# Optimization experiments

Hardware: AMD Instinct MI355X
Metric: run time of the kernel (lower is better)

The kernel has to match this reference:

```python
import jax, jax.numpy as jnp
import numpy as np

B, N, E, H, D, F = 2, 4096, 128, 8, 16, 512
EPS = 1e-6


def _rms_norm(x, w):
    xf = x.astype(jnp.float32)
    n = xf * jax.lax.rsqrt(jnp.mean(xf * xf, axis=-1, keepdims=True) + EPS)
    return n.astype(x.dtype) * w


def setup_inputs() -> dict:
    key = jax.random.key(0)
    ks = jax.random.split(key, 12)
    s = 1.0 / np.sqrt(E)
    sf = 1.0 / np.sqrt(F)
    coords = jax.random.uniform(ks[10], (B, N, 2))
    dis = jnp.sqrt(jnp.sum((coords[:, :, None, :] - coords[:, None, :, :]) ** 2, -1))
    dis = dis * (1.0 - jnp.eye(N))  # zero diagonal
    return {
        "input1": jax.random.normal(ks[0], (B, N, E), jnp.float32),
        "dis_matrix": dis.astype(jnp.float32),
        "Wq": jax.random.uniform(ks[1], (E, E), jnp.float32, -s, s),
        "Wk": jax.random.uniform(ks[2], (E, E), jnp.float32, -s, s),
        "Wv": jax.random.uniform(ks[3], (E, E), jnp.float32, -s, s),
        "alpha": jnp.float32(1.0),
        "ln1_w": jnp.ones((E,), jnp.float32),
        "ln2_w": jnp.ones((E,), jnp.float32),
        "Wcomb": jax.random.uniform(ks[4], (E, E), jnp.float32, -s, s),
        "W1": jax.random.uniform(ks[5], (F, E), jnp.float32, -s, s),
        "b1": jax.random.uniform(ks[6], (F,), jnp.float32, -s, s),
        "W2": jax.random.uniform(ks[7], (E, F), jnp.float32, -sf, sf),
        "b2": jax.random.uniform(ks[8], (E,), jnp.float32, -sf, sf),
    }


def _sparse_attention_afm(x, dis_matrix, Wq, Wk, Wv, alpha):
    # project and split heads: [B,N,E] -> [B,H,N,D]
    def heads(w):
        return (x @ w.T).reshape(B, N, H, D).transpose(0, 2, 1, 3)
    q, k, v = heads(Wq), heads(Wk), heads(Wv)
    log2n = jnp.float32(np.log2(N))
    dis_weight = jnp.exp(-alpha * log2n * dis_matrix)  # [B,N,N] (i,j)
    k_weight = jnp.exp(k)  # [B,H,N,D]
    w1 = jnp.einsum('bij,bhik->bhjk', dis_weight, k_weight * v)
    w2 = jnp.einsum('bij,bhik->bhjk', dis_weight, k_weight)
    out = jax.nn.sigmoid(q) * (w1 / w2)  # [B,H,N,D]
    return out.transpose(0, 2, 1, 3).reshape(B, N, E)


def reference(input1, dis_matrix, Wq, Wk, Wv, alpha, ln1_w, ln2_w, Wcomb, W1, b1, W2, b2):
    h = _rms_norm(input1, ln1_w)
    attn = _sparse_attention_afm(h, dis_matrix, Wq, Wk, Wv, alpha)
    out1 = input1 + attn @ Wcomb.T
    h2 = _rms_norm(out1, ln2_w)
    ffn = jax.nn.relu(h2 @ W1.T + b1) @ W2.T + b2
    return out1 + ffn
```

## Files before the change

### kernel.cpp

```cpp
#include <hip/hip_runtime.h>

#define NTOK 4096
#define BNROWS 8192
#define EDIM 128
#define FDIM 512

typedef __attribute__((ext_vector_type(8))) short bf16x8;
typedef __attribute__((ext_vector_type(4))) float f32x4;

__device__ __forceinline__ ushort f2bf(float x) {
    union { float f; unsigned u; } c; c.f = x;
    unsigned r = c.u + 0x7FFF + ((c.u >> 16) & 1);
    return (ushort)(r >> 16);
}

__launch_bounds__(256, 1)
__global__ void qkv_k(const float* __restrict__ input1, const float* __restrict__ ln1w,
                      const float* __restrict__ Wq, const float* __restrict__ Wk,
                      const float* __restrict__ Wv, const float* __restrict__ Wc,
                      const float* __restrict__ W1, const float* __restrict__ W2,
                      ushort* __restrict__ Wbf, float* __restrict__ sigq,
                      ushort* __restrict__ Mt) {
    const int bx = blockIdx.x, t = threadIdx.x;
    if (bx >= 256) {
        int off = (bx - 256) * 1024 + t * 4;
        const float* src; int o2;
        if (off < 16384)      { src = Wc; o2 = off; }
        else if (off < 81920) { src = W1; o2 = off - 16384; }
        else                  { src = W2; o2 = off - 81920; }
        float4 f = *(const float4*)(src + o2);
        ushort4 u; u.x = f2bf(f.x); u.y = f2bf(f.y); u.z = f2bf(f.z); u.w = f2bf(f.w);
        *(ushort4*)(Wbf + off) = u;
        return;
    }
    __shared__ ushort As[32 * 136];
    __shared__ ushort Bs[3][128 * 136];
    const int lane = t & 63, wv = t >> 6;
    const int m15 = lane & 15, quad = lane >> 4, kq = quad * 8;
    const int M0 = bx * 32;

    {
        const int ar = t >> 3, c0 = (t & 7) * 16;
        const float* xr = input1 + (size_t)(M0 + ar) * EDIM + c0;
        float4 x[4];
        float ss = 0.f;
#pragma unroll
        for (int i = 0; i < 4; ++i) {
            x[i] = ((const float4*)xr)[i];
            ss += x[i].x * x[i].x + x[i].y * x[i].y + x[i].z * x[i].z + x[i].w * x[i].w;
        }
        ss += __shfl_down(ss, 4, 8);
        ss += __shfl_down(ss, 2, 8);
        ss += __shfl_down(ss, 1, 8);
        ss = __shfl(ss, 0, 8);
        float rr = rsqrtf(ss * (1.0f / 128.0f) + 1e-6f);
#pragma unroll
        for (int i = 0; i < 4; ++i) {
            float4 wv4 = *(const float4*)&ln1w[c0 + i * 4];
            ushort4 o;
            o.x = f2bf(x[i].x * rr * wv4.x);
            o.y = f2bf(x[i].y * rr * wv4.y);
            o.z = f2bf(x[i].z * rr * wv4.z);
            o.w = f2bf(x[i].w * rr * wv4.w);
            *(ushort4*)&As[ar * 136 + c0 + i * 4] = o;
        }
    }
    {
        const int br = t >> 1, half = (t & 1) * 64;
        const float* srcs[3] = {Wq, Wk, Wv};
#pragma unroll
        for (int m = 0; m < 3; ++m) {
            const float* wsrc = srcs[m] + (size_t)br * 128 + half;
#pragma unroll
            for (int j = 0; j < 8; ++j) {
                float4 f0 = *(const float4*)(wsrc + j * 8);
                float4 f1 = *(const float4*)(wsrc + j * 8 + 4);
                bf16x8 u;
                u[0] = (short)f2bf(f0.x); u[1] = (short)f2bf(f0.y);
                u[2] = (short)f2bf(f0.z); u[3] = (short)f2bf(f0.w);
                u[4] = (short)f2bf(f1.x); u[5] = (short)f2bf(f1.y);
                u[6] = (short)f2bf(f1.z); u[7] = (short)f2bf(f1.w);
                *(bf16x8*)&Bs[m][br * 136 + half + j * 8] = u;
            }
        }
    }
    __syncthreads();

    f32x4 aq[2][2] = {}, ak[2][2] = {}, av[2][2] = {};
    const int c0w = wv * 32;
#pragma unroll
    for (int kc = 0; kc < 4; ++kc) {
        int ko = kc * 32 + kq;
        bf16x8 a0 = *(const bf16x8*)&As[m15 * 136 + ko];
        bf16x8 a1 = *(const bf16x8*)&As[(16 + m15) * 136 + ko];
#pragma unroll
        for (int ni = 0; ni < 2; ++ni) {
            int brow = (c0w + ni * 16 + m15) * 136 + ko;
            bf16x8 bq = *(const bf16x8*)&Bs[0][brow];
            bf16x8 bk = *(const bf16x8*)&Bs[1][brow];
            bf16x8 bv = *(const bf16x8*)&Bs[2][brow];
            aq[0][ni] = __builtin_amdgcn_mfma_f32_16x16x32_bf16(a0, bq, aq[0][ni], 0, 0, 0);
            aq[1][ni] = __builtin_amdgcn_mfma_f32_16x16x32_bf16(a1, bq, aq[1][ni], 0, 0, 0);
            ak[0][ni] = __builtin_amdgcn_mfma_f32_16x16x32_bf16(a0, bk, ak[0][ni], 0, 0, 0);
            ak[1][ni] = __builtin_amdgcn_mfma_f32_16x16x32_bf16(a1, bk, ak[1][ni], 0, 0, 0);
            av[0][ni] = __builtin_amdgcn_mfma_f32_16x16x32_bf16(a0, bv, av[0][ni], 0, 0, 0);
            av[1][ni] = __builtin_amdgcn_mfma_f32_16x16x32_bf16(a1, bv, av[1][ni], 0, 0, 0);
        }
    }
    const int b  = M0 >> 12;
    const int i0 = M0 & (NTOK - 1);
#pragma unroll
    for (int mi = 0; mi < 2; ++mi)
#pragma unroll
        for (int ni = 0; ni < 2; ++ni) {
            int e  = c0w + ni * 16 + m15;
            int ib = i0 + mi * 16 + quad * 4;
#pragma unroll
            for (int r = 0; r < 4; ++r)
                sigq[(size_t)(M0 + mi * 16 + quad * 4 + r) * EDIM + e] =
                    1.0f / (1.0f + __expf(-aq[mi][ni][r]));
            ushort4 pv, pk;
            float k0 = __expf(ak[mi][ni][0]); pv.x = f2bf(k0 * av[mi][ni][0]); pk.x = f2bf(k0);
            float k1 = __expf(ak[mi][ni][1]); pv.y = f2bf(k1 * av[mi][ni][1]); pk.y = f2bf(k1);
            float k2 = __expf(ak[mi][ni][2]); pv.z = f2bf(k2 * av[mi][ni][2]); pk.z = f2bf(k2);
            float k3 = __expf(ak[mi][ni][3]); pv.w = f2bf(k3 * av[mi][ni][3]); pk.w = f2bf(k3);
            *(ushort4*)&Mt[((size_t)b * 256 + e) * NTOK + ib]       = pv;
            *(ushort4*)&Mt[((size_t)b * 256 + 128 + e) * NTOK + ib] = pk;
        }
}

__launch_bounds__(256, 3)
__global__ void big_gemm_k(const float* __restrict__ dis, const float* __restrict__ alphap,
                           const ushort* __restrict__ Mt, float* __restrict__ P) {
    __shared__ ushort As[32 * 72];
    __shared__ ushort Bs[256 * 72];
    const int t = threadIdx.x, lane = t & 63, wv = t >> 6;
    const int m15 = lane & 15, quad = lane >> 4, kq = quad * 8;
    const int j0 = blockIdx.x * 32;
    const int b  = blockIdx.y;
    const int s  = blockIdx.z;
    const float coef = -alphap[0] * 12.0f;
    const float* disb = dis + (size_t)b * NTOK * NTOK;
    const ushort* Mtb = Mt + (size_t)b * 256 * NTOK;
    float* outp = P + ((size_t)(s * 2 + b) * NTOK + j0) * 256;

    f32x4 acc[2][4] = {};
    const int aj = t >> 3, ak = (t & 7) * 8;
    const int brow = t >> 3, bseg = (t & 7) * 8;
    const int k0 = s * (NTOK / 4);
    const int nIter = (NTOK / 4) / 64;

    float4 fa0, fa1;
    bf16x8 pb[8];
    {
        const float* ap = disb + (size_t)(j0 + aj) * NTOK + k0 + ak;
        fa0 = *(const float4*)ap; fa1 = *(const float4*)(ap + 4);
#pragma unroll
        for (int p = 0; p < 8; ++p)
            pb[p] = *(const bf16x8*)&Mtb[(size_t)(p * 32 + brow) * NTOK + k0 + bseg];
    }

    for (int it = 0; it < nIter; ++it) {
        bf16x8 a8;
        a8[0] = (short)f2bf(__expf(coef * fa0.x));
        a8[1] = (short)f2bf(__expf(coef * fa0.y));
        a8[2] = (short)f2bf(__expf(coef * fa0.z));
        a8[3] = (short)f2bf(__expf(coef * fa0.w));
        a8[4] = (short)f2bf(__expf(coef * fa1.x));
        a8[5] = (short)f2bf(__expf(coef * fa1.y));
        a8[6] = (short)f2bf(__expf(coef * fa1.z));
        a8[7] = (short)f2bf(__expf(coef * fa1.w));
        *(bf16x8*)&As[aj * 72 + ak] = a8;
#pragma unroll
        for (int p = 0; p < 8; ++p)
            *(bf16x8*)&Bs[(p * 32 + brow) * 72 + bseg] = pb[p];
        __syncthreads();
        if (it < nIter - 1) {
            int kn = k0 + (it + 1) * 64;
            const float* ap = disb + (size_t)(j0 + aj) * NTOK + kn + ak;
            fa0 = *(const float4*)ap; fa1 = *(const float4*)(ap + 4);
#pragma unroll
            for (int p = 0; p < 8; ++p)
                pb[p] = *(const bf16x8*)&Mtb[(size_t)(p * 32 + brow) * NTOK + kn + bseg];
        }
#pragma unroll
        for (int kh = 0; kh < 2; ++kh) {
            int ko = kh * 32 + kq;
            bf16x8 a0 = *(const bf16x8*)&As[m15 * 72 + ko];
            bf16x8 a1 = *(const bf16x8*)&As[(16 + m15) * 72 + ko];
#pragma unroll
            for (int ni = 0; ni < 4; ++ni) {
                bf16x8 bv = *(const bf16x8*)&Bs[(wv * 64 + ni * 16 + m15) * 72 + ko];
                acc[0][ni] = __builtin_amdgcn_mfma_f32_16x16x32_bf16(a0, bv, acc[0][ni], 0, 0, 0);
                acc[1][ni] = __builtin_amdgcn_mfma_f32_16x16x32_bf16(a1, bv, acc[1][ni], 0, 0, 0);
            }
        }
        __syncthreads();
    }
#pragma unroll
    for (int mi = 0; mi < 2; ++mi)
#pragma unroll
        for (int ni = 0; ni < 4; ++ni)
#pragma unroll
            for (int r = 0; r < 4; ++r) {
                int j = mi * 16 + quad * 4 + r;
                int c = wv * 64 + ni * 16 + m15;
                outp[(size_t)j * 256 + c] = acc[mi][ni][r];
            }
}

__launch_bounds__(256, 2)
__global__ void wcomb_rms2_k(const float* __restrict__ sigq, const float* __restrict__ P,
                             const ushort* __restrict__ Wbf,
                             const float* __restrict__ input1, const float* __restrict__ b2,
                             const float* __restrict__ ln2w,
                             float* __restrict__ outD, ushort* __restrict__ h2) {
    __shared__ ushort As[32 * 136];
    __shared__ ushort Bs[128 * 136];
    __shared__ float  O[32][132];
    const int t = threadIdx.x, lane = t & 63, wv = t >> 6;
    const int m15 = lane & 15, quad = lane >> 4, kq = quad * 8;
    const int M0 = blockIdx.x * 32;

    {
        const int ar = t >> 3, e0 = (t & 7) * 16;
        const int g = M0 + ar;
        const int b = g >> 12, j = g & (NTOK - 1);
        const float* sg = sigq + (size_t)g * 128 + e0;
        const float* Pg0 = P + ((size_t)(0 + b) * NTOK + j) * 256 + e0;
        const float* Pg1 = P + ((size_t)(2 + b) * NTOK + j) * 256 + e0;
        const float* Pg2 = P + ((size_t)(4 + b) * NTOK + j) * 256 + e0;
        const float* Pg3 = P + ((size_t)(6 + b) * NTOK + j) * 256 + e0;
#pragma unroll
        for (int i = 0; i < 4; ++i) {
            float4 s = *(const float4*)(sg + i * 4);
            float4 n0 = *(const float4*)(Pg0 + i * 4);
            float4 n1 = *(const float4*)(Pg1 + i * 4);
            float4 n2 = *(const float4*)(Pg2 + i * 4);
            float4 n3 = *(const float4*)(Pg3 + i * 4);
            float4 d0 = *(const float4*)(Pg0 + 128 + i * 4);
            float4 d1 = *(const float4*)(Pg1 + 128 + i * 4);
            float4 d2 = *(const float4*)(Pg2 + 128 + i * 4);
            float4 d3 = *(const float4*)(Pg3 + 128 + i * 4);
            ushort4 a;
            a.x = f2bf(s.x * (n0.x + n1.x + n2.x + n3.x) / (d0.x + d1.x + d2.x + d3.x));
            a.y = f2bf(s.y * (n0.y + n1.y + n2.y + n3.y) / (d0.y + d1.y + d2.y + d3.y));
            a.z = f2bf(s.z * (n0.z + n1.z + n2.z + n3.z) / (d0.z + d1.z + d2.z + d3.z));
            a.w = f2bf(s.w * (n0.w + n1.w + n2.w + n3.w) / (d0.w + d1.w + d2.w + d3.w));
            *(ushort4*)&As[ar * 136 + e0 + i * 4] = a;
        }
    }
    {
        const int br = t >> 1, half = (t & 1) * 64;
#pragma unroll
        for (int j = 0; j < 8; ++j)
            *(bf16x8*)&Bs[br * 136 + half + j * 8] =
                *(const bf16x8*)&Wbf[(size_t)br * 128 + half + j * 8];
    }
    __syncthreads();

    f32x4 acc[2][2] = {};
    const int c0w = wv * 32;
#pragma unroll
    for (int kc = 0; kc < 4; ++kc) {
        int ko = kc * 32 + kq;
        bf16x8 a0 = *(const bf16x8*)&As[m15 * 136 + ko];
        bf16x8 a1 = *(const bf16x8*)&As[(16 + m15) * 136 + ko];
        bf16x8 b0 = *(const bf16x8*)&Bs[(c0w + m15) * 136 + ko];
        bf16x8 b1 = *(const bf16x8*)&Bs[(c0w + 16 + m15) * 136 + ko];
        acc[0][0] = __builtin_amdgcn_mfma_f32_16x16x32_bf16(a0, b0, acc[0][0], 0, 0, 0);
        acc[0][1] = __builtin_amdgcn_mfma_f32_16x16x32_bf16(a0, b1, acc[0][1], 0, 0, 0);
        acc[1][0] = __builtin_amdgcn_mfma_f32_16x16x32_bf16(a1, b0, acc[1][0], 0, 0, 0);
        acc[1][1] = __builtin_amdgcn_mfma_f32_16x16x32_bf16(a1, b1, acc[1][1], 0, 0, 0);
    }
#pragma unroll
    for (int mi = 0; mi < 2; ++mi)
#pragma unroll
        for (int ni = 0; ni < 2; ++ni)
#pragma unroll
            for (int r = 0; r < 4; ++r) {
                int rl = mi * 16 + quad * 4 + r;
                int col = c0w + ni * 16 + m15;
                size_t off = (size_t)(M0 + rl) * 128 + col;
                float v = acc[mi][ni][r] + input1[off];
                O[rl][col] = v;
                outD[off] = v + b2[col];
            }
    __syncthreads();
    {
        const int row = t >> 3, seg = t & 7;
        float4 x[4];
        float ss = 0.f;
#pragma unroll
        for (int i = 0; i < 4; ++i) {
            x[i] = *(const float4*)&O[row][seg * 16 + i * 4];
            ss += x[i].x * x[i].x + x[i].y * x[i].y + x[i].z * x[i].z + x[i].w * x[i].w;
        }
        ss += __shfl_down(ss, 4, 8);
        ss += __shfl_down(ss, 2, 8);
        ss += __shfl_down(ss, 1, 8);
        ss = __shfl(ss, 0, 8);
        float rr = rsqrtf(ss * (1.0f / 128.0f) + 1e-6f);
        ushort* hp = h2 + (size_t)(M0 + row) * 128 + seg * 16;
#pragma unroll
        for (int i = 0; i < 4; ++i) {
            float4 wv4 = *(const float4*)&ln2w[seg * 16 + i * 4];
            ushort4 o;
            o.x = f2bf(x[i].x * rr * wv4.x);
            o.y = f2bf(x[i].y * rr * wv4.y);
            o.z = f2bf(x[i].z * rr * wv4.z);
            o.w = f2bf(x[i].w * rr * wv4.w);
            *(ushort4*)&hp[i * 4] = o;
        }
    }
}

__launch_bounds__(256, 2)
__global__ void ffn_k(const ushort* __restrict__ h2, const ushort* __restrict__ Wbf,
                      const float* __restrict__ b1, float* __restrict__ out) {
    __shared__ ushort As[32 * 136];
    __shared__ ushort Am[32 * 520];
    __shared__ ushort Bs[128 * 136];
    const int t = threadIdx.x, lane = t & 63, wv = t >> 6;
    const int m15 = lane & 15, quad = lane >> 4, kq = quad * 8;
    const int M0 = blockIdx.x * 32;
    const int c0w = wv * 32;
    const int br = t >> 1, half = (t & 1) * 64;
    const ushort* W1bf = Wbf + 16384;
    const ushort* W2bf = Wbf + 81920;

    {
        const int ar = t >> 3, a0 = (t & 7) * 16;
        *(bf16x8*)&As[ar * 136 + a0]     = *(const bf16x8*)&h2[(size_t)(M0 + ar) * 128 + a0];
        *(bf16x8*)&As[ar * 136 + a0 + 8] = *(const bf16x8*)&h2[(size_t)(M0 + ar) * 128 + a0 + 8];
    }
    for (int fc = 0; fc < 4; ++fc) {
        __syncthreads();
#pragma unroll
        for (int j = 0; j < 8; ++j)
            *(bf16x8*)&Bs[br * 136 + half + j * 8] =
                *(const bf16x8*)&W1bf[(size_t)(fc * 128 + br) * 128 + half + j * 8];
        __syncthreads();
        f32x4 acc[2][2] = {};
#pragma unroll
        for (int kc = 0; kc < 4; ++kc) {
            int ko = kc * 32 + kq;
            bf16x8 a0 = *(const bf16x8*)&As[m15 * 136 + ko];
            bf16x8 a1 = *(const bf16x8*)&As[(16 + m15) * 136 + ko];
            bf16x8 b0 = *(const bf16x8*)&Bs[(c0w + m15) * 136 + ko];
            bf16x8 b1v = *(const bf16x8*)&Bs[(c0w + 16 + m15) * 136 + ko];
            acc[0][0] = __builtin_amdgcn_mfma_f32_16x16x32_bf16(a0, b0, acc[0][0], 0, 0, 0);
            acc[0][1] = __builtin_amdgcn_mfma_f32_16x16x32_bf16(a0, b1v, acc[0][1], 0, 0, 0);
            acc[1][0] = __builtin_amdgcn_mfma_f32_16x16x32_bf16(a1, b0, acc[1][0], 0, 0, 0);
            acc[1][1] = __builtin_amdgcn_mfma_f32_16x16x32_bf16(a1, b1v, acc[1][1], 0, 0, 0);
        }
#pragma unroll
        for (int mi = 0; mi < 2; ++mi)
#pragma unroll
            for (int ni = 0; ni < 2; ++ni)
#pragma unroll
                for (int r = 0; r < 4; ++r) {
                    int row = mi * 16 + quad * 4 + r;
                    int col = c0w + ni * 16 + m15;
                    Am[row * 520 + fc * 128 + col] =
                        f2bf(fmaxf(acc[mi][ni][r] + b1[fc * 128 + col], 0.0f));
                }
    }
    f32x4 acc2[2][2] = {};
    for (int kc = 0; kc < 4; ++kc) {
        __syncthreads();
#pragma unroll
        for (int j = 0; j < 8; ++j)
            *(bf16x8*)&Bs[br * 136 + half + j * 8] =
                *(const bf16x8*)&W2bf[(size_t)br * 512 + kc * 128 + half + j * 8];
        __syncthreads();
#pragma unroll
        for (int kk = 0; kk < 4; ++kk) {
            int koA = kc * 128 + kk * 32 + kq;
            int koB = kk * 32 + kq;
            bf16x8 a0 = *(const bf16x8*)&Am[m15 * 520 + koA];
            bf16x8 a1 = *(const bf16x8*)&Am[(16 + m15) * 520 + koA];
            bf16x8 b0 = *(const bf16x8*)&Bs[(c0w + m15) * 136 + koB];
            bf16x8 b1v = *(const bf16x8*)&Bs[(c0w + 16 + m15) * 136 + koB];
            acc2[0][0] = __builtin_amdgcn_mfma_f32_16x16x32_bf16(a0, b0, acc2[0][0], 0, 0, 0);
            acc2[0][1] = __builtin_amdgcn_mfma_f32_16x16x32_bf16(a0, b1v, acc2[0][1], 0, 0, 0);
            acc2[1][0] = __builtin_amdgcn_mfma_f32_16x16x32_bf16(a1, b0, acc2[1][0], 0, 0, 0);
            acc2[1][1] = __builtin_amdgcn_mfma_f32_16x16x32_bf16(a1, b1v, acc2[1][1], 0, 0, 0);
        }
    }
#pragma unroll
    for (int mi = 0; mi < 2; ++mi)
#pragma unroll
        for (int ni = 0; ni < 2; ++ni)
#pragma unroll
            for (int r = 0; r < 4; ++r) {
                int row = M0 + mi * 16 + quad * 4 + r;
                int col = c0w + ni * 16 + m15;
                size_t off = (size_t)row * 128 + col;
                out[off] += acc2[mi][ni][r];
            }
}

extern "C" void kernel_launch(void* const* d_in, const int* in_sizes, int n_in,
                              void* d_out, int out_size, void* d_ws, size_t ws_size,
                              hipStream_t stream) {
    const float* input1 = (const float*)d_in[0];
    const float* dis    = (const float*)d_in[1];
    const float* Wq     = (const float*)d_in[2];
    const float* Wk     = (const float*)d_in[3];
    const float* Wv     = (const float*)d_in[4];
    const float* alpha  = (const float*)d_in[5];
    const float* ln1    = (const float*)d_in[6];
    const float* ln2    = (const float*)d_in[7];
    const float* Wcomb  = (const float*)d_in[8];
    const float* W1     = (const float*)d_in[9];
    const float* b1     = (const float*)d_in[10];
    const float* W2     = (const float*)d_in[11];
    const float* b2     = (const float*)d_in[12];
    float* out = (float*)d_out;

    char* w8 = (char*)d_ws;
    ushort* Wbf  = (ushort*)(w8);
    float*  sigq = (float*)(w8 + (4u << 20));
    ushort* Mt   = (ushort*)(w8 + (8u << 20));
    ushort* h2   = (ushort*)(w8 + (12u << 20));
    float*  P    = (float*)(w8 + (16u << 20));

    qkv_k<<<dim3(400), 256, 0, stream>>>(input1, ln1, Wq, Wk, Wv, Wcomb, W1, W2,
                                         Wbf, sigq, Mt);
    big_gemm_k<<<dim3(128, 2, 4), 256, 0, stream>>>(dis, alpha, Mt, P);
    wcomb_rms2_k<<<dim3(256), 256, 0, stream>>>(sigq, P, Wbf, input1, b2, ln2, out, h2);
    ffn_k<<<dim3(256), 256, 0, stream>>>(h2, Wbf, b1, out);
}
```

Measured before the change: 280.0 us.

## Split QKV over output halves, remap big GEMM grid, fuse wcomb/rms2 with FFN

The QKV projection kernel now splits each 32-row tile across two blocks by output-feature half, doubling the grid and halving shared memory per block. The big dis GEMM uses a flattened 1D grid with a custom block-to-tile mapping, nontemporal loads for the streaming distance matrix and nontemporal stores for partials. The Wcomb+RMSNorm kernel is fused with the FFN kernel, keeping h2 in shared memory and writing the output once instead of a read-modify-write. These changes aim to cut a kernel launch, global round trips and cache pollution, at the cost of extra syncs and shared-memory aliasing.

```diff
diff --git a/kernel.cpp b/kernel.cpp
--- a/kernel.cpp
+++ b/kernel.cpp
@@ -14,7 +14,7 @@
     return (ushort)(r >> 16);
 }
 
-__launch_bounds__(256, 1)
+__launch_bounds__(256, 2)
 __global__ void qkv_k(const float* __restrict__ input1, const float* __restrict__ ln1w,
                       const float* __restrict__ Wq, const float* __restrict__ Wk,
                       const float* __restrict__ Wv, const float* __restrict__ Wc,
@@ -22,8 +22,8 @@
                       ushort* __restrict__ Wbf, float* __restrict__ sigq,
                       ushort* __restrict__ Mt) {
     const int bx = blockIdx.x, t = threadIdx.x;
-    if (bx >= 256) {
-        int off = (bx - 256) * 1024 + t * 4;
+    if (bx >= 512) {
+        int off = (bx - 512) * 1024 + t * 4;
         const float* src; int o2;
         if (off < 16384)      { src = Wc; o2 = off; }
         else if (off < 81920) { src = W1; o2 = off - 16384; }
@@ -34,10 +34,11 @@
         return;
     }
     __shared__ ushort As[32 * 136];
-    __shared__ ushort Bs[3][128 * 136];
+    __shared__ ushort Bs[3][64 * 136];
     const int lane = t & 63, wv = t >> 6;
     const int m15 = lane & 15, quad = lane >> 4, kq = quad * 8;
-    const int M0 = bx * 32;
+    const int M0 = (bx >> 1) * 32;
+    const int eh = (bx & 1) * 64;
 
     {
         const int ar = t >> 3, c0 = (t & 7) * 16;
@@ -66,13 +67,13 @@
         }
     }
     {
-        const int br = t >> 1, half = (t & 1) * 64;
+        const int br = t >> 2, koff = (t & 3) * 32;
         const float* srcs[3] = {Wq, Wk, Wv};
 #pragma unroll
         for (int m = 0; m < 3; ++m) {
-            const float* wsrc = srcs[m] + (size_t)br * 128 + half;
-#pragma unroll
-            for (int j = 0; j < 8; ++j) {
+            const float* wsrc = srcs[m] + (size_t)(eh + br) * 128 + koff;
+#pragma unroll
+            for (int j = 0; j < 4; ++j) {
                 float4 f0 = *(const float4*)(wsrc + j * 8);
                 float4 f1 = *(const float4*)(wsrc + j * 8 + 4);
                 bf16x8 u;
@@ -80,53 +81,48 @@
                 u[2] = (short)f2bf(f0.z); u[3] = (short)f2bf(f0.w);
                 u[4] = (short)f2bf(f1.x); u[5] = (short)f2bf(f1.y);
                 u[6] = (short)f2bf(f1.z); u[7] = (short)f2bf(f1.w);
-                *(bf16x8*)&Bs[m][br * 136 + half + j * 8] = u;
+                *(bf16x8*)&Bs[m][br * 136 + koff + j * 8] = u;
             }
         }
     }
     __syncthreads();
 
-    f32x4 aq[2][2] = {}, ak[2][2] = {}, av[2][2] = {};
-    const int c0w = wv * 32;
+    f32x4 aq[2] = {}, ak[2] = {}, av[2] = {};
+    const int c0w = wv * 16;
 #pragma unroll
     for (int kc = 0; kc < 4; ++kc) {
         int ko = kc * 32 + kq;
         bf16x8 a0 = *(const bf16x8*)&As[m15 * 136 + ko];
         bf16x8 a1 = *(const bf16x8*)&As[(16 + m15) * 136 + ko];
-#pragma unroll
-        for (int ni = 0; ni < 2; ++ni) {
-            int brow = (c0w + ni * 16 + m15) * 136 + ko;
-            bf16x8 bq = *(const bf16x8*)&Bs[0][brow];
-            bf16x8 bk = *(const bf16x8*)&Bs[1][brow];
-            bf16x8 bv = *(const bf16x8*)&Bs[2][brow];
-            aq[0][ni] = __builtin_amdgcn_mfma_f32_16x16x32_bf16(a0, bq, aq[0][ni], 0, 0, 0);
-            aq[1][ni] = __builtin_amdgcn_mfma_f32_16x16x32_bf16(a1, bq, aq[1][ni], 0, 0, 0);
-            ak[0][ni] = __builtin_amdgcn_mfma_f32_16x16x32_bf16(a0, bk, ak[0][ni], 0, 0, 0);
-            ak[1][ni] = __builtin_amdgcn_mfma_f32_16x16x32_bf16(a1, bk, ak[1][ni], 0, 0, 0);
-            av[0][ni] = __builtin_amdgcn_mfma_f32_16x16x32_bf16(a0, bv, av[0][ni], 0, 0, 0);
-            av[1][ni] = __builtin_amdgcn_mfma_f32_16x16x32_bf16(a1, bv, av[1][ni], 0, 0, 0);
-        }
+        int brow = (c0w + m15) * 136 + ko;
+        bf16x8 bq = *(const bf16x8*)&Bs[0][brow];
+        bf16x8 bk = *(const bf16x8*)&Bs[1][brow];
+        bf16x8 bv = *(const bf16x8*)&Bs[2][brow];
+        aq[0] = __builtin_amdgcn_mfma_f32_16x16x32_bf16(a0, bq, aq[0], 0, 0, 0);
+        aq[1] = __builtin_amdgcn_mfma_f32_16x16x32_bf16(a1, bq, aq[1], 0, 0, 0);
+        ak[0] = __builtin_amdgcn_mfma_f32_16x16x32_bf16(a0, bk, ak[0], 0, 0, 0);
+        ak[1] = __builtin_amdgcn_mfma_f32_16x16x32_bf16(a1, bk, ak[1], 0, 0, 0);
+        av[0] = __builtin_amdgcn_mfma_f32_16x16x32_bf16(a0, bv, av[0], 0, 0, 0);
+        av[1] = __builtin_amdgcn_mfma_f32_16x16x32_bf16(a1, bv, av[1], 0, 0, 0);
     }
     const int b  = M0 >> 12;
     const int i0 = M0 & (NTOK - 1);
-#pragma unroll
-    for (int mi = 0; mi < 2; ++mi)
-#pragma unroll
-        for (int ni = 0; ni < 2; ++ni) {
-            int e  = c0w + ni * 16 + m15;
-            int ib = i0 + mi * 16 + quad * 4;
-#pragma unroll
-            for (int r = 0; r < 4; ++r)
-                sigq[(size_t)(M0 + mi * 16 + quad * 4 + r) * EDIM + e] =
-                    1.0f / (1.0f + __expf(-aq[mi][ni][r]));
-            ushort4 pv, pk;
-            float k0 = __expf(ak[mi][ni][0]); pv.x = f2bf(k0 * av[mi][ni][0]); pk.x = f2bf(k0);
-            float k1 = __expf(ak[mi][ni][1]); pv.y = f2bf(k1 * av[mi][ni][1]); pk.y = f2bf(k1);
-            float k2 = __expf(ak[mi][ni][2]); pv.z = f2bf(k2 * av[mi][ni][2]); pk.z = f2bf(k2);
-            float k3 = __expf(ak[mi][ni][3]); pv.w = f2bf(k3 * av[mi][ni][3]); pk.w = f2bf(k3);
-            *(ushort4*)&Mt[((size_t)b * 256 + e) * NTOK + ib]       = pv;
-            *(ushort4*)&Mt[((size_t)b * 256 + 128 + e) * NTOK + ib] = pk;
-        }
+    const int e  = eh + c0w + m15;
+#pragma unroll
+    for (int mi = 0; mi < 2; ++mi) {
+        int ib = i0 + mi * 16 + quad * 4;
+#pragma unroll
+        for (int r = 0; r < 4; ++r)
+            sigq[(size_t)(M0 + mi * 16 + quad * 4 + r) * EDIM + e] =
+                1.0f / (1.0f + __expf(-aq[mi][r]));
+        ushort4 pv, pk;
+        float k0 = __expf(ak[mi][0]); pv.x = f2bf(k0 * av[mi][0]); pk.x = f2bf(k0);
+        float k1 = __expf(ak[mi][1]); pv.y = f2bf(k1 * av[mi][1]); pk.y = f2bf(k1);
+        float k2 = __expf(ak[mi][2]); pv.z = f2bf(k2 * av[mi][2]); pk.z = f2bf(k2);
+        float k3 = __expf(ak[mi][3]); pv.w = f2bf(k3 * av[mi][3]); pk.w = f2bf(k3);
+        *(ushort4*)&Mt[((size_t)b * 256 + e) * NTOK + ib]       = pv;
+        *(ushort4*)&Mt[((size_t)b * 256 + 128 + e) * NTOK + ib] = pk;
+    }
 }
 
 __launch_bounds__(256, 3)
@@ -134,11 +130,13 @@
                            const ushort* __restrict__ Mt, float* __restrict__ P) {
     __shared__ ushort As[32 * 72];
     __shared__ ushort Bs[256 * 72];
+    const int id = blockIdx.x;
+    const int b = (id >> 2) & 1;
+    const int tile = (id & 3) | ((id >> 3) << 2);
+    const int j0 = (tile & 127) * 32;
+    const int s  = tile >> 7;
     const int t = threadIdx.x, lane = t & 63, wv = t >> 6;
     const int m15 = lane & 15, quad = lane >> 4, kq = quad * 8;
-    const int j0 = blockIdx.x * 32;
-    const int b  = blockIdx.y;
-    const int s  = blockIdx.z;
     const float coef = -alphap[0] * 12.0f;
     const float* disb = dis + (size_t)b * NTOK * NTOK;
     const ushort* Mtb = Mt + (size_t)b * 256 * NTOK;
@@ -150,11 +148,12 @@
     const int k0 = s * (NTOK / 4);
     const int nIter = (NTOK / 4) / 64;
 
-    float4 fa0, fa1;
+    f32x4 fa0, fa1;
     bf16x8 pb[8];
     {
-        const float* ap = disb + (size_t)(j0 + aj) * NTOK + k0 + ak;
-        fa0 = *(const float4*)ap; fa1 = *(const float4*)(ap + 4);
+        const f32x4* ap = (const f32x4*)(disb + (size_t)(j0 + aj) * NTOK + k0 + ak);
+        fa0 = __builtin_nontemporal_load(ap);
+        fa1 = __builtin_nontemporal_load(ap + 1);
 #pragma unroll
         for (int p = 0; p < 8; ++p)
             pb[p] = *(const bf16x8*)&Mtb[(size_t)(p * 32 + brow) * NTOK + k0 + bseg];
@@ -162,14 +161,14 @@
 
     for (int it = 0; it < nIter; ++it) {
         bf16x8 a8;
-        a8[0] = (short)f2bf(__expf(coef * fa0.x));
-        a8[1] = (short)f2bf(__expf(coef * fa0.y));
-        a8[2] = (short)f2bf(__expf(coef * fa0.z));
-        a8[3] = (short)f2bf(__expf(coef * fa0.w));
-        a8[4] = (short)f2bf(__expf(coef * fa1.x));
-        a8[5] = (short)f2bf(__expf(coef * fa1.y));
-        a8[6] = (short)f2bf(__expf(coef * fa1.z));
-        a8[7] = (short)f2bf(__expf(coef * fa1.w));
+        a8[0] = (short)f2bf(__expf(coef * fa0[0]));
+        a8[1] = (short)f2bf(__expf(coef * fa0[1]));
+        a8[2] = (short)f2bf(__expf(coef * fa0[2]));
+        a8[3] = (short)f2bf(__expf(coef * fa0[3]));
+        a8[4] = (short)f2bf(__expf(coef * fa1[0]));
+        a8[5] = (short)f2bf(__expf(coef * fa1[1]));
+        a8[6] = (short)f2bf(__expf(coef * fa1[2]));
+        a8[7] = (short)f2bf(__expf(coef * fa1[3]));
         *(bf16x8*)&As[aj * 72 + ak] = a8;
 #pragma unroll
         for (int p = 0; p < 8; ++p)
@@ -177,8 +176,9 @@
         __syncthreads();
         if (it < nIter - 1) {
             int kn = k0 + (it + 1) * 64;
-            const float* ap = disb + (size_t)(j0 + aj) * NTOK + kn + ak;
-            fa0 = *(const float4*)ap; fa1 = *(const float4*)(ap + 4);
+            const f32x4* ap = (const f32x4*)(disb + (size_t)(j0 + aj) * NTOK + kn + ak);
+            fa0 = __builtin_nontemporal_load(ap);
+            fa1 = __builtin_nontemporal_load(ap + 1);
 #pragma unroll
             for (int p = 0; p < 8; ++p)
                 pb[p] = *(const bf16x8*)&Mtb[(size_t)(p * 32 + brow) * NTOK + kn + bseg];
@@ -205,22 +205,25 @@
             for (int r = 0; r < 4; ++r) {
                 int j = mi * 16 + quad * 4 + r;
                 int c = wv * 64 + ni * 16 + m15;
-                outp[(size_t)j * 256 + c] = acc[mi][ni][r];
+                __builtin_nontemporal_store(acc[mi][ni][r], &outp[(size_t)j * 256 + c]);
             }
 }
 
 __launch_bounds__(256, 2)
-__global__ void wcomb_rms2_k(const float* __restrict__ sigq, const float* __restrict__ P,
-                             const ushort* __restrict__ Wbf,
-                             const float* __restrict__ input1, const float* __restrict__ b2,
-                             const float* __restrict__ ln2w,
-                             float* __restrict__ outD, ushort* __restrict__ h2) {
+__global__ void wcomb_ffn_k(const float* __restrict__ sigq, const float* __restrict__ P,
+                            const ushort* __restrict__ Wbf,
+                            const float* __restrict__ input1, const float* __restrict__ b1,
+                            const float* __restrict__ b2, const float* __restrict__ ln2w,
+                            float* __restrict__ outD) {
     __shared__ ushort As[32 * 136];
     __shared__ ushort Bs[128 * 136];
-    __shared__ float  O[32][132];
+    __shared__ ushort Am[32 * 520];
+    float* O = (float*)Am;
     const int t = threadIdx.x, lane = t & 63, wv = t >> 6;
     const int m15 = lane & 15, quad = lane >> 4, kq = quad * 8;
     const int M0 = blockIdx.x * 32;
+    const int c0w = wv * 32;
+    const int br = t >> 1, half = (t & 1) * 64;
 
     {
         const int ar = t >> 3, e0 = (t & 7) * 16;
@@ -233,7 +236,7 @@
         const float* Pg3 = P + ((size_t)(6 + b) * NTOK + j) * 256 + e0;
 #pragma unroll
         for (int i = 0; i < 4; ++i) {
-            float4 s = *(const float4*)(sg + i * 4);
+            float4 sv = *(const float4*)(sg + i * 4);
             float4 n0 = *(const float4*)(Pg0 + i * 4);
             float4 n1 = *(const float4*)(Pg1 + i * 4);
             float4 n2 = *(const float4*)(Pg2 + i * 4);
@@ -243,15 +246,14 @@
             float4 d2 = *(const float4*)(Pg2 + 128 + i * 4);
             float4 d3 = *(const float4*)(Pg3 + 128 + i * 4);
             ushort4 a;
-            a.x = f2bf(s.x * (n0.x + n1.x + n2.x + n3.x) / (d0.x + d1.x + d2.x + d3.x));
-            a.y = f2bf(s.y * (n0.y + n1.y + n2.y + n3.y) / (d0.y + d1.y + d2.y + d3.y));
-            a.z = f2bf(s.z * (n0.z + n1.z + n2.z + n3.z) / (d0.z + d1.z + d2.z + d3.z));
-            a.w = f2bf(s.w * (n0.w + n1.w + n2.w + n3.w) / (d0.w + d1.w + d2.w + d3.w));
+            a.x = f2bf(sv.x * (n0.x + n1.x + n2.x + n3.x) / (d0.x + d1.x + d2.x + d3.x));
+            a.y = f2bf(sv.y * (n0.y + n1.y + n2.y + n3.y) / (d0.y + d1.y + d2.y + d3.y));
+            a.z = f2bf(sv.z * (n0.z + n1.z + n2.z + n3.z) / (d0.z + d1.z + d2.z + d3.z));
+            a.w = f2bf(sv.w * (n0.w + n1.w + n2.w + n3.w) / (d0.w + d1.w + d2.w + d3.w));
             *(ushort4*)&As[ar * 136 + e0 + i * 4] = a;
         }
     }
     {
-        const int br = t >> 1, half = (t & 1) * 64;
 #pragma unroll
         for (int j = 0; j < 8; ++j)
             *(bf16x8*)&Bs[br * 136 + half + j * 8] =
@@ -260,32 +262,35 @@
     __syncthreads();
 
     f32x4 acc[2][2] = {};
-    const int c0w = wv * 32;
 #pragma unroll
     for (int kc = 0; kc < 4; ++kc) {
         int ko = kc * 32 + kq;
         bf16x8 a0 = *(const bf16x8*)&As[m15 * 136 + ko];
         bf16x8 a1 = *(const bf16x8*)&As[(16 + m15) * 136 + ko];
         bf16x8 b0 = *(const bf16x8*)&Bs[(c0w + m15) * 136 + ko];
-        bf16x8 b1 = *(const bf16x8*)&Bs[(c0w + 16 + m15) * 136 + ko];
+        bf16x8 b1v = *(const bf16x8*)&Bs[(c0w + 16 + m15) * 136 + ko];
         acc[0][0] = __builtin_amdgcn_mfma_f32_16x16x32_bf16(a0, b0, acc[0][0], 0, 0, 0);
-        acc[0][1] = __builtin_amdgcn_mfma_f32_16x16x32_bf16(a0, b1, acc[0][1], 0, 0, 0);
+        acc[0][1] = __builtin_amdgcn_mfma_f32_16x16x32_bf16(a0, b1v, acc[0][1], 0, 0, 0);
         acc[1][0] = __builtin_amdgcn_mfma_f32_16x16x32_bf16(a1, b0, acc[1][0], 0, 0, 0);
-        acc[1][1] = __builtin_amdgcn_mfma_f32_16x16x32_bf16(a1, b1, acc[1][1], 0, 0, 0);
-    }
+        acc[1][1] = __builtin_amdgcn_mfma_f32_16x16x32_bf16(a1, b1v, acc[1][1], 0, 0, 0);
+    }
+    float vout[2][2][4];
+    __syncthreads();
 #pragma unroll
     for (int mi = 0; mi < 2; ++mi)
 #pragma unroll
-        for (int ni = 0; ni < 2; ++ni)
+        for (int ni = 0; ni < 2; ++ni) {
+            int col = c0w + ni * 16 + m15;
+            float bb = b2[col];
 #pragma unroll
             for (int r = 0; r < 4; ++r) {
                 int rl = mi * 16 + quad * 4 + r;
-                int col = c0w + ni * 16 + m15;
                 size_t off = (size_t)(M0 + rl) * 128 + col;
                 float v = acc[mi][ni][r] + input1[off];
-                O[rl][col] = v;
-                outD[off] = v + b2[col];
+                O[rl * 132 + col] = v;
+                vout[mi][ni][r] = v + bb;
             }
+        }
     __syncthreads();
     {
         const int row = t >> 3, seg = t & 7;
@@ -293,7 +298,7 @@
         float ss = 0.f;
 #pragma unroll
         for (int i = 0; i < 4; ++i) {
-            x[i] = *(const float4*)&O[row][seg * 16 + i * 4];
+            x[i] = *(const float4*)&O[row * 132 + seg * 16 + i * 4];
             ss += x[i].x * x[i].x + x[i].y * x[i].y + x[i].z * x[i].z + x[i].w * x[i].w;
         }
         ss += __shfl_down(ss, 4, 8);
@@ -301,7 +306,6 @@
         ss += __shfl_down(ss, 1, 8);
         ss = __shfl(ss, 0, 8);
         float rr = rsqrtf(ss * (1.0f / 128.0f) + 1e-6f);
-        ushort* hp = h2 + (size_t)(M0 + row) * 128 + seg * 16;
 #pragma unroll
         for (int i = 0; i < 4; ++i) {
             float4 wv4 = *(const float4*)&ln2w[seg * 16 + i * 4];
@@ -310,30 +314,11 @@
             o.y = f2bf(x[i].y * rr * wv4.y);
             o.z = f2bf(x[i].z * rr * wv4.z);
             o.w = f2bf(x[i].w * rr * wv4.w);
-            *(ushort4*)&hp[i * 4] = o;
-        }
-    }
-}
-
-__launch_bounds__(256, 2)
-__global__ void ffn_k(const ushort* __restrict__ h2, const ushort* __restrict__ Wbf,
-                      const float* __restrict__ b1, float* __restrict__ out) {
-    __shared__ ushort As[32 * 136];
-    __shared__ ushort Am[32 * 520];
-    __shared__ ushort Bs[128 * 136];
-    const int t = threadIdx.x, lane = t & 63, wv = t >> 6;
-    const int m15 = lane & 15, quad = lane >> 4, kq = quad * 8;
-    const int M0 = blockIdx.x * 32;
-    const int c0w = wv * 32;
-    const int br = t >> 1, half = (t & 1) * 64;
+            *(ushort4*)&As[row * 136 + seg * 16 + i * 4] = o;
+        }
+    }
     const ushort* W1bf = Wbf + 16384;
     const ushort* W2bf = Wbf + 81920;
-
-    {
-        const int ar = t >> 3, a0 = (t & 7) * 16;
-        *(bf16x8*)&As[ar * 136 + a0]     = *(const bf16x8*)&h2[(size_t)(M0 + ar) * 128 + a0];
-        *(bf16x8*)&As[ar * 136 + a0 + 8] = *(const bf16x8*)&h2[(size_t)(M0 + ar) * 128 + a0 + 8];
-    }
     for (int fc = 0; fc < 4; ++fc) {
         __syncthreads();
 #pragma unroll
@@ -341,7 +326,7 @@
             *(bf16x8*)&Bs[br * 136 + half + j * 8] =
                 *(const bf16x8*)&W1bf[(size_t)(fc * 128 + br) * 128 + half + j * 8];
         __syncthreads();
-        f32x4 acc[2][2] = {};
+        f32x4 ac[2][2] = {};
 #pragma unroll
         for (int kc = 0; kc < 4; ++kc) {
             int ko = kc * 32 + kq;
@@ -349,11 +334,12 @@
             bf16x8 a1 = *(const bf16x8*)&As[(16 + m15) * 136 + ko];
             bf16x8 b0 = *(const bf16x8*)&Bs[(c0w + m15) * 136 + ko];
             bf16x8 b1v = *(const bf16x8*)&Bs[(c0w + 16 + m15) * 136 + ko];
-            acc[0][0] = __builtin_amdgcn_mfma_f32_16x16x32_bf16(a0, b0, acc[0][0], 0, 0, 0);
-            acc[0][1] = __builtin_amdgcn_mfma_f32_16x16x32_bf16(a0, b1v, acc[0][1], 0, 0, 0);
-            acc[1][0] = __builtin_amdgcn_mfma_f32_16x16x32_bf16(a1, b0, acc[1][0], 0, 0, 0);
-            acc[1][1] = __builtin_amdgcn_mfma_f32_16x16x32_bf16(a1, b1v, acc[1][1], 0, 0, 0);
-        }
+            ac[0][0] = __builtin_amdgcn_mfma_f32_16x16x32_bf16(a0, b0, ac[0][0], 0, 0, 0);
+            ac[0][1] = __builtin_amdgcn_mfma_f32_16x16x32_bf16(a0, b1v, ac[0][1], 0, 0, 0);
+            ac[1][0] = __builtin_amdgcn_mfma_f32_16x16x32_bf16(a1, b0, ac[1][0], 0, 0, 0);
+            ac[1][1] = __builtin_amdgcn_mfma_f32_16x16x32_bf16(a1, b1v, ac[1][1], 0, 0, 0);
+        }
+        __syncthreads();
 #pragma unroll
         for (int mi = 0; mi < 2; ++mi)
 #pragma unroll
@@ -363,7 +349,7 @@
                     int row = mi * 16 + quad * 4 + r;
                     int col = c0w + ni * 16 + m15;
                     Am[row * 520 + fc * 128 + col] =
-                        f2bf(fmaxf(acc[mi][ni][r] + b1[fc * 128 + col], 0.0f));
+                        f2bf(fmaxf(ac[mi][ni][r] + b1[fc * 128 + col], 0.0f));
                 }
     }
     f32x4 acc2[2][2] = {};
@@ -396,8 +382,7 @@
             for (int r = 0; r < 4; ++r) {
                 int row = M0 + mi * 16 + quad * 4 + r;
                 int col = c0w + ni * 16 + m15;
-                size_t off = (size_t)row * 128 + col;
-                out[off] += acc2[mi][ni][r];
+                outD[(size_t)row * 128 + col] = vout[mi][ni][r] + acc2[mi][ni][r];
             }
 }
 
@@ -423,12 +408,10 @@
     ushort* Wbf  = (ushort*)(w8);
     float*  sigq = (float*)(w8 + (4u << 20));
     ushort* Mt   = (ushort*)(w8 + (8u << 20));
-    ushort* h2   = (ushort*)(w8 + (12u << 20));
     float*  P    = (float*)(w8 + (16u << 20));
 
-    qkv_k<<<dim3(400), 256, 0, stream>>>(input1, ln1, Wq, Wk, Wv, Wcomb, W1, W2,
+    qkv_k<<<dim3(656), 256, 0, stream>>>(input1, ln1, Wq, Wk, Wv, Wcomb, W1, W2,
                                          Wbf, sigq, Mt);
-    big_gemm_k<<<dim3(128, 2, 4), 256, 0, stream>>>(dis, alpha, Mt, P);
-    wcomb_rms2_k<<<dim3(256), 256, 0, stream>>>(sigq, P, Wbf, input1, b2, ln2, out, h2);
-    ffn_k<<<dim3(256), 256, 0, stream>>>(h2, Wbf, b1, out);
+    big_gemm_k<<<dim3(1024), 256, 0, stream>>>(dis, alpha, Mt, P);
+    wcomb_ffn_k<<<dim3(256), 256, 0, stream>>>(sigq, P, Wbf, input1, b1, b2, ln2, out);
 }
```

After: 281.0 us. No clear change (+0.4%).
